# Kernel optimization log

Hardware: AMD Instinct MI355X
Metric: run time of the kernel (lower is better)

## Reference

```python
import jax, jax.numpy as jnp
import numpy as np

P, D, K, E, ITERS, THRESH, NCLS = 16, 384, 16, 8, 10, 0.9, 1000


def _forward(x, pw, pb, ln_g, ln_b, pos, qw, qb, kw, kb, vw, vb,
             ew, eb, nw, nb, m1w, m1b, m2w, m2b, fbw, fbb, fgw, fgb, cw, cb):
    B, C, H, W = x.shape
    Hp, Wp = H // P, W // P
    # patch embedding: conv(k=s=P) == reshape + matmul; (c, ph, pw) ordering matches conv weight layout
    xp = x.reshape(B, C, Hp, P, Wp, P).transpose(0, 2, 4, 1, 3, 5).reshape(B, Hp * Wp, C * P * P)
    patches = xp @ pw + pb                                    # [B, N, D]
    # layer norm (eps=1e-5)
    mu = patches.mean(-1, keepdims=True)
    var = patches.var(-1, keepdims=True)
    pn = (patches - mu) / jnp.sqrt(var + 1e-5) * ln_g + ln_b
    # k-means (Lloyd, fixed iters, deterministic evenly-spaced init)
    N = pn.shape[1]
    init_idx = jnp.linspace(0, N - 1, K).astype(jnp.int32)
    centers0 = pn[:, init_idx]                                # [B, K, D]
    pn_sq = jnp.sum(pn * pn, -1)                              # [B, N]

    def kstep(centers, _):
        d2 = (pn_sq[:, :, None]
              - 2.0 * jnp.einsum('bnd,bkd->bnk', pn, centers)
              + jnp.sum(centers * centers, -1)[:, None, :])   # [B, N, K]
        oh = jax.nn.one_hot(jnp.argmin(d2, -1), K, dtype=pn.dtype)
        counts = oh.sum(1)                                    # [B, K]
        new = jnp.einsum('bnk,bnd->bkd', oh, pn) / jnp.maximum(counts, 1.0)[:, :, None]
        new = jnp.where(counts[:, :, None] > 0, new, centers)
        return new, None

    clusters, _ = jax.lax.scan(kstep, centers0, None, length=ITERS)  # [B, K, D]
    # attention over clusters
    clusters = clusters + pos
    Q = clusters @ qw + qb
    Kt = clusters @ kw + kb
    V = clusters @ vw + vb
    attn = jax.nn.softmax(jnp.einsum('bqd,bkd->bqk', Q, Kt) / jnp.sqrt(jnp.float32(D)), -1)
    clusters = jnp.einsum('bqk,bkd->bqd', attn, V)
    # hypergraph laplacian
    hw = jax.nn.softmax(clusters @ ew + eb, axis=1)           # [B, K, E], softmax over nodes
    Dd = hw.sum(1)                                            # [B, E]
    Hm = hw.transpose(0, 2, 1)                                # [B, E, K]
    M = (Dd ** -0.5)[:, :, None] * Hm                         # D^{-1/2} H
    L = jnp.eye(E, dtype=clusters.dtype) - jnp.einsum('bek,bfk->bef', M, Hm)  # [B, E, E]
    L = jnp.pad(L, ((0, 0), (0, K - E), (0, K - E)))          # pad to [B, K, K]
    clusters = jnp.einsum('bij,bjd->bid', L, clusters)
    clusters = clusters @ nw + nb
    # non-linear propagation MLP (exact GELU, torch default)
    clusters = jax.nn.gelu(clusters @ m1w + m1b, approximate=False) @ m2w + m2b
    # adaptive node collapse: mask from ORIGINAL clusters, sequential in-place merges
    nrm = jnp.maximum(jnp.linalg.norm(clusters, axis=-1, keepdims=True), 1e-12)
    nc = clusters / nrm
    sim = jnp.einsum('bqd,bkd->bqk', nc, nc)
    mask_any = jnp.any(sim > THRESH, axis=0)                  # [K, K]: merge pair if ANY batch exceeds
    for i in range(K):                                        # small fixed K; matches sequential torch loop
        for j in range(i + 1, K):
            cond = mask_any[i, j]
            merged = (clusters[:, i] + clusters[:, j]) * 0.5
            clusters = clusters.at[:, i].set(jnp.where(cond, merged, clusters[:, i]))
            clusters = clusters.at[:, j].set(jnp.where(cond, merged, clusters[:, j]))
    # feedback modulation
    g = clusters.mean(1)                                      # [B, D]
    fb = g @ fbw + fbb
    gate = jax.nn.sigmoid(g @ fgw + fgb)                      # [B, 1]
    clusters = clusters + fb[:, None, :] * gate[:, None, :]
    return clusters.reshape(B, -1) @ cw + cb                  # [B, num_classes]


def setup_inputs() -> dict:
    key = jax.random.key(0)
    ks = jax.random.split(key, 16)
    Wm = lambda k, *s: jax.random.normal(k, s, jnp.float32) * 0.02
    z = lambda *s: jnp.zeros(s, jnp.float32)
    return {
        'x': jax.random.normal(ks[0], (128, 3, 224, 224), jnp.float32),
        'pw': Wm(ks[1], 3 * P * P, D), 'pb': z(D),
        'ln_g': jnp.ones((D,), jnp.float32), 'ln_b': z(D),
        'pos': Wm(ks[2], K, D),
        'qw': Wm(ks[3], D, D), 'qb': z(D),
        'kw': Wm(ks[4], D, D), 'kb': z(D),
        'vw': Wm(ks[5], D, D), 'vb': z(D),
        'ew': Wm(ks[6], D, E), 'eb': z(E),
        'nw': Wm(ks[7], D, D), 'nb': z(D),
        'm1w': Wm(ks[8], D, D), 'm1b': z(D),
        'm2w': Wm(ks[9], D, D), 'm2b': z(D),
        'fbw': Wm(ks[10], D, D), 'fbb': z(D),
        'fgw': Wm(ks[11], D, 1), 'fgb': z(1),
        'cw': Wm(ks[12], D * K, NCLS), 'cb': z(NCLS),
    }


def reference(x, pw, pb, ln_g, ln_b, pos, qw, qb, kw, kb, vw, vb,
              ew, eb, nw, nb, m1w, m1b, m2w, m2b, fbw, fbb, fgw, fgb, cw, cb):
    return _forward(x, pw, pb, ln_g, ln_b, pos, qw, qb, kw, kb, vw, vb,
                    ew, eb, nw, nb, m1w, m1b, m2w, m2b, fbw, fbb, fgw, fgb, cw, cb)
```

## Files before the change

kernel.cpp:

```cpp
#include <hip/hip_runtime.h>
#include <math.h>

#define NBATCH 128
#define NPTS   196
#define DIN    768
#define DM     384
#define KCL    16
#define NEXP   8
#define NITER  10
#define NCLS   1000

__global__ __launch_bounds__(256) void init_kernel(const float* __restrict__ cb,
                                                   float* __restrict__ out,
                                                   int* __restrict__ mask) {
    int idx = blockIdx.x * 256 + threadIdx.x;
    if (idx < NBATCH * NCLS) {
        out[idx] = cb[idx % NCLS];
    } else if (idx < NBATCH * NCLS + 256) {
        mask[idx - NBATCH * NCLS] = 0;
    }
}

#define BKP 16
__global__ __launch_bounds__(512, 4) void patch_ln_kernel(
        const float* __restrict__ x, const float* __restrict__ pw,
        const float* __restrict__ pb, const float* __restrict__ lng,
        const float* __restrict__ lnb, float* __restrict__ pn,
        float* __restrict__ pnsq) {
    __shared__ float As[BKP * 68];
    __shared__ float Ws[BKP * DM];
    const int tid = threadIdx.x;
    const int m0  = blockIdx.x * 64;
    const int rg  = tid >> 6;
    const int cg  = tid & 63;
    const int lr = (tid & 255) >> 2, kq = tid & 3;
    const int m  = m0 + lr;
    const int bi = m / NPTS, n = m - bi * NPTS;
    const int nh = n / 14, nwp = n - nh * 14;
    const float* xb = x + (size_t)bi * 150528 + (size_t)(nh * 16) * 224 + nwp * 16;

    float acc[8][6];
#pragma unroll
    for (int r = 0; r < 8; ++r)
#pragma unroll
        for (int j = 0; j < 6; ++j) acc[r][j] = 0.f;

    const float4* pw4 = (const float4*)pw;
    for (int kc = 0; kc < DIN; kc += BKP) {
        if (tid < 256) {
            int k = kc + kq * 4;
            int c = k >> 8, py = (k >> 4) & 15, px = k & 15;
            float4 xv = *(const float4*)(xb + c * 50176 + py * 224 + px);
            As[(kq * 4 + 0) * 68 + lr] = xv.x;
            As[(kq * 4 + 1) * 68 + lr] = xv.y;
            As[(kq * 4 + 2) * 68 + lr] = xv.z;
            As[(kq * 4 + 3) * 68 + lr] = xv.w;
        }
#pragma unroll
        for (int t = 0; t < 3; ++t) {
            int s = tid + t * 512;
            ((float4*)Ws)[s] = pw4[kc * 96 + s];
        }
        __syncthreads();
#pragma unroll 4
        for (int kk = 0; kk < BKP; ++kk) {
            float a[8];
            *(float4*)&a[0] = *(const float4*)&As[kk * 68 + rg * 8];
            *(float4*)&a[4] = *(const float4*)&As[kk * 68 + rg * 8 + 4];
            float w[6];
#pragma unroll
            for (int j = 0; j < 6; ++j) w[j] = Ws[kk * DM + cg + 64 * j];
#pragma unroll
            for (int r = 0; r < 8; ++r)
#pragma unroll
                for (int j = 0; j < 6; ++j) acc[r][j] += a[r] * w[j];
        }
        __syncthreads();
    }

    float gvv[6], bvv[6], pbv[6];
#pragma unroll
    for (int j = 0; j < 6; ++j) {
        pbv[j] = pb[cg + 64 * j];
        gvv[j] = lng[cg + 64 * j];
        bvv[j] = lnb[cg + 64 * j];
    }
#pragma unroll
    for (int r = 0; r < 8; ++r) {
        float vloc[6];
        float s = 0.f;
#pragma unroll
        for (int j = 0; j < 6; ++j) { vloc[j] = acc[r][j] + pbv[j]; s += vloc[j]; }
#pragma unroll
        for (int off = 32; off >= 1; off >>= 1) s += __shfl_xor(s, off);
        float mu = s * (1.0f / DM);
        float q = 0.f;
#pragma unroll
        for (int j = 0; j < 6; ++j) { float dd = vloc[j] - mu; q += dd * dd; }
#pragma unroll
        for (int off = 32; off >= 1; off >>= 1) q += __shfl_xor(q, off);
        float rstd = rsqrtf(q * (1.0f / DM) + 1e-5f);
        float ov[6];
        float ssq = 0.f;
#pragma unroll
        for (int j = 0; j < 6; ++j) {
            float p = (vloc[j] - mu) * rstd * gvv[j] + bvv[j];
            ov[j] = p; ssq += p * p;
        }
#pragma unroll
        for (int off = 32; off >= 1; off >>= 1) ssq += __shfl_xor(ssq, off);
        int mr = m0 + rg * 8 + r;
        float* dst = pn + (size_t)mr * DM + cg;
#pragma unroll
        for (int j = 0; j < 6; ++j) dst[64 * j] = ov[j];
        if (cg == 0) pnsq[mr] = ssq;
    }
}

__global__ __launch_bounds__(256) void kmeans_init_kernel(
        const float* __restrict__ pn, float* __restrict__ cent,
        float* __restrict__ csq, int* __restrict__ cnt) {
    const int b = blockIdx.x, tid = threadIdx.x;
    const float* pnb = pn + (size_t)b * NPTS * DM;
    float* cb = cent + (size_t)b * KCL * DM;
    for (int i = tid; i < KCL * DM / 4; i += 256) {
        int k = i / (DM / 4), d4 = i - k * (DM / 4);
        ((float4*)cb)[i] = ((const float4*)(pnb + (size_t)(13 * k) * DM))[d4];
    }
    if (tid < 128) {
        int k = tid >> 3, sub = tid & 7;
        const float* row = pnb + (size_t)(13 * k) * DM + sub * 48;
        float ss = 0.f;
        for (int d = 0; d < 48; d += 4) {
            float4 v = *(const float4*)(row + d);
            ss += v.x * v.x + v.y * v.y + v.z * v.z + v.w * v.w;
        }
#pragma unroll
        for (int off = 4; off >= 1; off >>= 1) ss += __shfl_xor(ss, off);
        if (sub == 0) csq[b * KCL + k] = ss;
    }
    if (tid < KCL) cnt[b * KCL + tid] = 0;
}

__global__ __launch_bounds__(256) void kmeans_assign_kernel(
        const float* __restrict__ pn, const float* __restrict__ pnsq,
        const float* __restrict__ cent, const float* __restrict__ csq,
        int* __restrict__ asn, int* __restrict__ cnt) {
    __shared__ float cs[KCL * DM];
    __shared__ float cq[KCL];
    const int b = blockIdx.y, tile = blockIdx.x, tid = threadIdx.x;
    const float* cb = cent + (size_t)b * KCL * DM;
    for (int i = tid; i < KCL * DM / 4; i += 256)
        ((float4*)cs)[i] = ((const float4*)cb)[i];
    if (tid < KCL) cq[tid] = csq[b * KCL + tid];
    __syncthreads();

    const int p = tid >> 3, sub = tid & 7;
    const int n = tile * 32 + p;
    if (n >= NPTS) return;
    const float4* prow = (const float4*)(pn + ((size_t)b * NPTS + n) * DM);

    float acc[KCL];
#pragma unroll
    for (int k = 0; k < KCL; ++k) acc[k] = 0.f;
#pragma unroll 2
    for (int i = 0; i < 12; ++i) {
        const int d4 = sub + 8 * i;
        float4 pv = prow[d4];
#pragma unroll
        for (int k = 0; k < KCL; ++k) {
            const float4 c = *(const float4*)&cs[k * DM + d4 * 4];
            acc[k] += pv.x * c.x + pv.y * c.y + pv.z * c.z + pv.w * c.w;
        }
    }
#pragma unroll
    for (int k = 0; k < KCL; ++k) {
        float a = acc[k];
        a += __shfl_xor(a, 1);
        a += __shfl_xor(a, 2);
        a += __shfl_xor(a, 4);
        acc[k] = a;
    }
    if (sub == 0) {
        const float mp = pnsq[b * NPTS + n];
        float best = (mp - 2.0f * acc[0]) + cq[0];
        int bk = 0;
#pragma unroll
        for (int k = 1; k < KCL; ++k) {
            float v = (mp - 2.0f * acc[k]) + cq[k];
            if (v < best) { best = v; bk = k; }
        }
        asn[b * NPTS + n] = bk;
        atomicAdd(&cnt[b * KCL + bk], 1);
    }
}

__global__ __launch_bounds__(256) void kmeans_update_kernel(
        const float* __restrict__ pn, const int* __restrict__ asn,
        int* __restrict__ cnt, float* __restrict__ cent,
        float* __restrict__ csq) {
    __shared__ unsigned long long msk[4];
    __shared__ float red[4];
    const int b = blockIdx.y, k = blockIdx.x, tid = threadIdx.x;

    int a = -1;
    if (tid < NPTS) a = asn[b * NPTS + tid];
    unsigned long long bal = __ballot(a == k);
    if ((tid & 63) == 0) msk[tid >> 6] = bal;
    __syncthreads();

    const int c = cnt[b * KCL + k];
    float sx = 0.f, sy = 0.f;
    const float* pnb = pn + (size_t)b * NPTS * DM + 2 * tid;
    if (tid < 192) {
#pragma unroll
        for (int w = 0; w < 4; ++w) {
            unsigned long long m = msk[w];
            while (m) {
                int nn = w * 64 + (int)__builtin_ctzll(m);
                m &= m - 1;
                float2 v = *(const float2*)(pnb + (size_t)nn * DM);
                sx += v.x; sy += v.y;
            }
        }
    }
    float* cr = cent + ((size_t)b * KCL + k) * DM + 2 * tid;
    float nx = 0.f, ny = 0.f;
    if (tid < 192) {
        if (c > 0) {
            float inv = 1.0f / (float)c;
            nx = sx * inv; ny = sy * inv;
        } else {
            nx = cr[0]; ny = cr[1];
        }
        cr[0] = nx; cr[1] = ny;
    }
    float ss = nx * nx + ny * ny;
#pragma unroll
    for (int off = 32; off >= 1; off >>= 1) ss += __shfl_xor(ss, off);
    if ((tid & 63) == 0) red[tid >> 6] = ss;
    __syncthreads();
    if (tid == 0) {
        csq[b * KCL + k] = red[0] + red[1] + red[2] + red[3];
        cnt[b * KCL + k] = 0;
    }
}

__global__ __launch_bounds__(256) void kmeans_finalize_kernel(
        float* __restrict__ cent, const float* __restrict__ pos) {
    int i = blockIdx.x * 256 + threadIdx.x;
    int within = i % (KCL * DM / 4);
    float4 cv = ((const float4*)cent)[i];
    float4 pv = ((const float4*)pos)[within];
    cv.x += pv.x; cv.y += pv.y; cv.z += pv.z; cv.w += pv.w;
    ((float4*)cent)[i] = cv;
}

__global__ __launch_bounds__(256) void gemm_qkv_kernel(
        const float* __restrict__ A,
        const float* __restrict__ qw, const float* __restrict__ kw,
        const float* __restrict__ vw,
        const float* __restrict__ qb, const float* __restrict__ kb,
        const float* __restrict__ vb,
        float* __restrict__ Q, float* __restrict__ K, float* __restrict__ V) {
    __shared__ float As[32 * 32];
    __shared__ float Ws[3][32 * 128];
    const int n0 = blockIdx.x * 128;
    const int m0 = blockIdx.y * 32;
    const int tid = threadIdx.x;
    const int rg = tid >> 5, cg = tid & 31;
    const int arow = tid >> 3, akg = tid & 7;
    const float* W[3] = {qw, kw, vw};

    float acc[3][4][4];
#pragma unroll
    for (int g = 0; g < 3; ++g)
#pragma unroll
        for (int r = 0; r < 4; ++r)
#pragma unroll
            for (int j = 0; j < 4; ++j) acc[g][r][j] = 0.f;

    for (int kc = 0; kc < DM; kc += 32) {
        float4 av = *(const float4*)(A + (size_t)(m0 + arow) * DM + kc + akg * 4);
        As[(akg * 4 + 0) * 32 + arow] = av.x;
        As[(akg * 4 + 1) * 32 + arow] = av.y;
        As[(akg * 4 + 2) * 32 + arow] = av.z;
        As[(akg * 4 + 3) * 32 + arow] = av.w;
#pragma unroll
        for (int g = 0; g < 3; ++g)
#pragma unroll
            for (int t = 0; t < 4; ++t) {
                int s = tid + t * 256;
                int kk = s >> 5, c4i = s & 31;
                *(float4*)&Ws[g][kk * 128 + c4i * 4] =
                    *(const float4*)(W[g] + (size_t)(kc + kk) * DM + n0 + c4i * 4);
            }
        __syncthreads();
#pragma unroll 8
        for (int kk = 0; kk < 32; ++kk) {
            float4 a = *(const float4*)&As[kk * 32 + rg * 4];
            float ar[4] = {a.x, a.y, a.z, a.w};
#pragma unroll
            for (int g = 0; g < 3; ++g) {
                float4 w = *(const float4*)&Ws[g][kk * 128 + cg * 4];
                float wr[4] = {w.x, w.y, w.z, w.w};
#pragma unroll
                for (int r = 0; r < 4; ++r)
#pragma unroll
                    for (int j = 0; j < 4; ++j) acc[g][r][j] += ar[r] * wr[j];
            }
        }
        __syncthreads();
    }
    const float* B[3] = {qb, kb, vb};
    float* O[3] = {Q, K, V};
#pragma unroll
    for (int g = 0; g < 3; ++g) {
        float4 bv = *(const float4*)(B[g] + n0 + cg * 4);
        float bvr[4] = {bv.x, bv.y, bv.z, bv.w};
#pragma unroll
        for (int r = 0; r < 4; ++r) {
            float o[4];
#pragma unroll
            for (int j = 0; j < 4; ++j) o[j] = acc[g][r][j] + bvr[j];
            *(float4*)(O[g] + (size_t)(m0 + rg * 4 + r) * DM + n0 + cg * 4) =
                *(float4*)&o[0];
        }
    }
}

template <int ACT>
__global__ __launch_bounds__(256) void gemm_kernel(
        const float* __restrict__ A, const float* __restrict__ W,
        const float* __restrict__ bias, float* __restrict__ out,
        int M, int N, int Kd) {
    __shared__ float As[32 * 32];
    __shared__ float Ws[32 * 128];
    const int n0 = blockIdx.x * 128;
    const int m0 = blockIdx.y * 32;
    const int tid = threadIdx.x;
    const int rg = tid >> 5, cg = tid & 31;
    const int arow = tid >> 3, akg = tid & 7;
    float acc[4][4];
#pragma unroll
    for (int r = 0; r < 4; ++r)
#pragma unroll
        for (int j = 0; j < 4; ++j) acc[r][j] = 0.f;

    for (int kc = 0; kc < Kd; kc += 32) {
        float4 av = *(const float4*)(A + (size_t)(m0 + arow) * Kd + kc + akg * 4);
        As[(akg * 4 + 0) * 32 + arow] = av.x;
        As[(akg * 4 + 1) * 32 + arow] = av.y;
        As[(akg * 4 + 2) * 32 + arow] = av.z;
        As[(akg * 4 + 3) * 32 + arow] = av.w;
#pragma unroll
        for (int t = 0; t < 4; ++t) {
            int s = tid + t * 256;
            int kk = s >> 5, c4i = s & 31;
            *(float4*)&Ws[kk * 128 + c4i * 4] =
                *(const float4*)(W + (size_t)(kc + kk) * N + n0 + c4i * 4);
        }
        __syncthreads();
#pragma unroll 16
        for (int kk = 0; kk < 32; ++kk) {
            float4 a = *(const float4*)&As[kk * 32 + rg * 4];
            float4 w = *(const float4*)&Ws[kk * 128 + cg * 4];
            float ar[4] = {a.x, a.y, a.z, a.w};
            float wr[4] = {w.x, w.y, w.z, w.w};
#pragma unroll
            for (int r = 0; r < 4; ++r)
#pragma unroll
                for (int j = 0; j < 4; ++j) acc[r][j] += ar[r] * wr[j];
        }
        __syncthreads();
    }
    float4 bv = *(const float4*)(bias + n0 + cg * 4);
    float bvr[4] = {bv.x, bv.y, bv.z, bv.w};
#pragma unroll
    for (int r = 0; r < 4; ++r) {
        float o[4];
#pragma unroll
        for (int j = 0; j < 4; ++j) {
            float v = acc[r][j] + bvr[j];
            if (ACT == 1) v = 0.5f * v * (1.0f + erff(v * 0.70710678118654752440f));
            o[j] = v;
        }
        *(float4*)(out + (size_t)(m0 + rg * 4 + r) * N + n0 + cg * 4) = *(float4*)&o[0];
    }
}

__global__ __launch_bounds__(256) void attn_spectral_kernel(
        const float* __restrict__ Qg, const float* __restrict__ Kg,
        const float* __restrict__ Vg, const float* __restrict__ ew,
        const float* __restrict__ eb, float* __restrict__ c2) {
    __shared__ float Qs[KCL * 388];
    __shared__ float Ks[KCL * 388];
    __shared__ float ewt[NEXP * 388];
    __shared__ float Ss[KCL * 17];
    __shared__ float hws[KCL * 9];
    __shared__ float rds[NEXP];
    __shared__ float Ls[NEXP * NEXP];
    const int b = blockIdx.x, tid = threadIdx.x;
    for (int idx = tid; idx < KCL * DM; idx += 256) {
        int i = idx / DM, d = idx - i * DM;
        size_t g = (size_t)b * KCL * DM + idx;
        Qs[i * 388 + d] = Qg[g];
        Ks[i * 388 + d] = Kg[g];
    }
    for (int idx = tid; idx < DM * NEXP; idx += 256) {
        int d = idx >> 3, e = idx & 7;
        ewt[e * 388 + d] = ew[idx];
    }
    __syncthreads();
    {
        int i = tid >> 4, j = tid & 15;
        float acc = 0.f;
        for (int d = 0; d < DM; d += 4) {
            float4 q = *(const float4*)&Qs[i * 388 + d];
            float4 k = *(const float4*)&Ks[j * 388 + d];
            acc += q.x * k.x + q.y * k.y + q.z * k.z + q.w * k.w;
        }
        float s = acc / sqrtf((float)DM);
        float mx = s;
#pragma unroll
        for (int off = 8; off >= 1; off >>= 1) mx = fmaxf(mx, __shfl_xor(mx, off));
        float p = expf(s - mx);
        float sm = p;
#pragma unroll
        for (int off = 8; off >= 1; off >>= 1) sm += __shfl_xor(sm, off);
        Ss[i * 17 + j] = p / sm;
    }
    __syncthreads();
    for (int idx = tid; idx < KCL * DM; idx += 256) {
        int i = idx / DM, d = idx - i * DM;
        Ks[i * 388 + d] = Vg[(size_t)b * KCL * DM + idx];
    }
    __syncthreads();
    for (int idx = tid; idx < KCL * DM; idx += 256) {
        int i = idx / DM, d = idx - i * DM;
        float acc = 0.f;
#pragma unroll
        for (int j = 0; j < KCL; ++j) acc += Ss[i * 17 + j] * Ks[j * 388 + d];
        Qs[i * 388 + d] = acc;
    }
    __syncthreads();
    if (tid < 128) {
        int e = tid >> 4, i = tid & 15;
        float l = 0.f;
        for (int d4 = 0; d4 < DM / 4; ++d4) {
            float4 q = *(const float4*)&Qs[i * 388 + d4 * 4];
            float4 w = *(const float4*)&ewt[e * 388 + d4 * 4];
            l += q.x * w.x + q.y * w.y + q.z * w.z + q.w * w.w;
        }
        l += eb[e];
        float mx = l;
#pragma unroll
        for (int off = 8; off >= 1; off >>= 1) mx = fmaxf(mx, __shfl_xor(mx, off));
        float p = expf(l - mx);
        float sm = p;
#pragma unroll
        for (int off = 8; off >= 1; off >>= 1) sm += __shfl_xor(sm, off);
        float h = p / sm;
        hws[i * 9 + e] = h;
        float sd = h;
#pragma unroll
        for (int off = 8; off >= 1; off >>= 1) sd += __shfl_xor(sd, off);
        if (i == 0) rds[e] = 1.0f / sqrtf(sd);
    }
    __syncthreads();
    if (tid < 64) {
        int e = tid >> 3, f = tid & 7;
        float gsum = 0.f;
#pragma unroll
        for (int k = 0; k < KCL; ++k) gsum += hws[k * 9 + e] * hws[k * 9 + f];
        Ls[e * 8 + f] = ((e == f) ? 1.0f : 0.0f) - rds[e] * gsum;
    }
    __syncthreads();
    for (int idx = tid; idx < KCL * DM; idx += 256) {
        int i = idx / DM, d = idx - i * DM;
        float acc = 0.f;
        if (i < NEXP) {
#pragma unroll
            for (int j = 0; j < NEXP; ++j) acc += Ls[i * 8 + j] * Qs[j * 388 + d];
        }
        c2[(size_t)b * KCL * DM + idx] = acc;
    }
}

__global__ __launch_bounds__(256) void simmask_kernel(const float* __restrict__ c4,
                                                      int* __restrict__ mask) {
    __shared__ float Cs[KCL * 388];
    __shared__ float rns[KCL];
    const int b = blockIdx.x, tid = threadIdx.x;
    for (int idx = tid; idx < KCL * DM; idx += 256) {
        int i = idx / DM, d = idx - i * DM;
        Cs[i * 388 + d] = c4[(size_t)b * KCL * DM + idx];
    }
    __syncthreads();
    {
        int i = tid >> 4, s = tid & 15;
        float ss = 0.f;
        for (int t = 0; t < 24; ++t) { float v = Cs[i * 388 + s + 16 * t]; ss += v * v; }
#pragma unroll
        for (int off = 8; off >= 1; off >>= 1) ss += __shfl_xor(ss, off);
        if (s == 0) rns[i] = 1.0f / fmaxf(sqrtf(ss), 1e-12f);
    }
    __syncthreads();
    for (int idx = tid; idx < KCL * DM; idx += 256) {
        int i = idx / DM, d = idx - i * DM;
        Cs[i * 388 + d] *= rns[i];
    }
    __syncthreads();
    {
        int i = tid >> 4, j = tid & 15;
        if (j > i) {
            float dp = 0.f;
            for (int d = 0; d < DM; d += 4) {
                float4 a = *(const float4*)&Cs[i * 388 + d];
                float4 c = *(const float4*)&Cs[j * 388 + d];
                dp += a.x * c.x + a.y * c.y + a.z * c.z + a.w * c.w;
            }
            if (dp > 0.9f) atomicOr(&mask[i * KCL + j], 1);
        }
    }
}

__global__ __launch_bounds__(256) void merge_fb_kernel(
        const float* __restrict__ c4, const int* __restrict__ mask,
        const float* __restrict__ fbw, const float* __restrict__ fbb,
        const float* __restrict__ fgw, const float* __restrict__ fgb,
        float* __restrict__ c5) {
    __shared__ int   mk[256];
    __shared__ float gs[DM];
    __shared__ float wred[3];
    __shared__ float gatev;
    const int b = blockIdx.x, tid = threadIdx.x;
    mk[tid] = mask[tid];
    const bool act = tid < 192;
    const int t = tid;
    float2 v[KCL];
    if (act) {
#pragma unroll
        for (int i = 0; i < KCL; ++i)
            v[i] = *(const float2*)(c4 + (size_t)b * KCL * DM + i * DM + 2 * t);
    }
    __syncthreads();
    if (act) {
#pragma unroll
        for (int i = 0; i < KCL; ++i)
#pragma unroll
            for (int j = i + 1; j < KCL; ++j)
                if (mk[i * KCL + j]) {
                    float mx = 0.5f * (v[i].x + v[j].x);
                    float my = 0.5f * (v[i].y + v[j].y);
                    v[i].x = mx; v[i].y = my; v[j].x = mx; v[j].y = my;
                }
    }
    float2 gv = {0.f, 0.f};
    if (act) {
#pragma unroll
        for (int i = 0; i < KCL; ++i) { gv.x += v[i].x; gv.y += v[i].y; }
        gv.x *= 0.0625f; gv.y *= 0.0625f;
        gs[2 * t] = gv.x; gs[2 * t + 1] = gv.y;
    }
    float pg = act ? (gv.x * fgw[2 * t] + gv.y * fgw[2 * t + 1]) : 0.f;
#pragma unroll
    for (int off = 32; off >= 1; off >>= 1) pg += __shfl_xor(pg, off);
    if (act && (tid & 63) == 0) wred[tid >> 6] = pg;
    __syncthreads();
    if (tid == 0) {
        float d = wred[0] + wred[1] + wred[2] + fgb[0];
        gatev = 1.0f / (1.0f + expf(-d));
    }
    __syncthreads();
    if (act) {
        float fx = fbb[2 * t], fy = fbb[2 * t + 1];
        for (int j = 0; j < DM; ++j) {
            float gj = gs[j];
            const float2 w = *(const float2*)(fbw + (size_t)j * DM + 2 * t);
            fx += gj * w.x; fy += gj * w.y;
        }
        float gt = gatev;
#pragma unroll
        for (int i = 0; i < KCL; ++i) {
            float2 o = {v[i].x + fx * gt, v[i].y + fy * gt};
            *(float2*)(c5 + (size_t)b * KCL * DM + i * DM + 2 * t) = o;
        }
    }
}

__global__ __launch_bounds__(256) void cls_kernel(const float* __restrict__ A,
                                                  const float* __restrict__ Wt,
                                                  float* __restrict__ out) {
    __shared__ float As[32 * 32];
    __shared__ float Ws[32 * 128];
    const int n0 = blockIdx.x * 128;
    const int m0 = blockIdx.y * 32;
    const int k0 = blockIdx.z * 768;
    const int tid = threadIdx.x;
    const int rg = tid >> 5, cg = tid & 31;
    const int arow = tid >> 3, akg = tid & 7;
    float acc[4][4];
#pragma unroll
    for (int r = 0; r < 4; ++r)
#pragma unroll
        for (int j = 0; j < 4; ++j) acc[r][j] = 0.f;

    for (int kc = k0; kc < k0 + 768; kc += 32) {
        float4 av = *(const float4*)(A + (size_t)(m0 + arow) * (KCL * DM) + kc + akg * 4);
        As[(akg * 4 + 0) * 32 + arow] = av.x;
        As[(akg * 4 + 1) * 32 + arow] = av.y;
        As[(akg * 4 + 2) * 32 + arow] = av.z;
        As[(akg * 4 + 3) * 32 + arow] = av.w;
#pragma unroll
        for (int ti = 0; ti < 4; ++ti) {
            int s = tid + ti * 256;
            int kk = s >> 5, c4i = s & 31;
            int col = n0 + c4i * 4;
            float4 wv = make_float4(0.f, 0.f, 0.f, 0.f);
            if (col < NCLS) wv = *(const float4*)(Wt + (size_t)(kc + kk) * NCLS + col);
            *(float4*)&Ws[kk * 128 + c4i * 4] = wv;
        }
        __syncthreads();
#pragma unroll 16
        for (int kk = 0; kk < 32; ++kk) {
            float4 a = *(const float4*)&As[kk * 32 + rg * 4];
            float4 w = *(const float4*)&Ws[kk * 128 + cg * 4];
            float ar[4] = {a.x, a.y, a.z, a.w};
            float wr[4] = {w.x, w.y, w.z, w.w};
#pragma unroll
            for (int r = 0; r < 4; ++r)
#pragma unroll
                for (int j = 0; j < 4; ++j) acc[r][j] += ar[r] * wr[j];
        }
        __syncthreads();
    }
    int col = n0 + cg * 4;
    if (col < NCLS) {
#pragma unroll
        for (int r = 0; r < 4; ++r) {
            int row = m0 + rg * 4 + r;
#pragma unroll
            for (int j = 0; j < 4; ++j)
                atomicAdd(&out[(size_t)row * NCLS + col + j], acc[r][j]);
        }
    }
}

extern "C" void kernel_launch(void* const* d_in, const int* in_sizes, int n_in,
                              void* d_out, int out_size, void* d_ws, size_t ws_size,
                              hipStream_t stream) {
    const float* x   = (const float*)d_in[0];
    const float* pw  = (const float*)d_in[1];
    const float* pb  = (const float*)d_in[2];
    const float* lng = (const float*)d_in[3];
    const float* lnb = (const float*)d_in[4];
    const float* pos = (const float*)d_in[5];
    const float* qw  = (const float*)d_in[6];
    const float* qb  = (const float*)d_in[7];
    const float* kw  = (const float*)d_in[8];
    const float* kb  = (const float*)d_in[9];
    const float* vw  = (const float*)d_in[10];
    const float* vb  = (const float*)d_in[11];
    const float* ew  = (const float*)d_in[12];
    const float* eb  = (const float*)d_in[13];
    const float* nw  = (const float*)d_in[14];
    const float* nb  = (const float*)d_in[15];
    const float* m1w = (const float*)d_in[16];
    const float* m1b = (const float*)d_in[17];
    const float* m2w = (const float*)d_in[18];
    const float* m2b = (const float*)d_in[19];
    const float* fbw = (const float*)d_in[20];
    const float* fbb = (const float*)d_in[21];
    const float* fgw = (const float*)d_in[22];
    const float* fgb = (const float*)d_in[23];
    const float* cw  = (const float*)d_in[24];
    const float* cb  = (const float*)d_in[25];
    float* out = (float*)d_out;
    float* ws  = (float*)d_ws;

    float* pn_   = ws;
    float* pnsq_ = ws + 9633792;
    float* c0_   = ws + 9658880;
    float* Q_    = ws + 10445312;
    float* K_    = ws + 11231744;
    float* V_    = ws + 12018176;
    float* c2_   = ws + 12804608;
    int*   mask_ = (int*)(ws + 13591040);
    float* csq_  = ws + 13591296;
    int*   cnt_  = (int*)(ws + 13593344);
    int*   asn_  = (int*)(ws + 13595392);
    float* cent_ = c0_;
    float* c3_ = Q_;
    float* h_  = K_;
    float* c4_ = V_;
    float* c5_ = c0_;

    init_kernel<<<501, 256, 0, stream>>>(cb, out, mask_);
    patch_ln_kernel<<<392, 512, 0, stream>>>(x, pw, pb, lng, lnb, pn_, pnsq_);

    kmeans_init_kernel<<<NBATCH, 256, 0, stream>>>(pn_, cent_, csq_, cnt_);
    for (int it = 0; it < NITER; ++it) {
        kmeans_assign_kernel<<<dim3(7, NBATCH), 256, 0, stream>>>(
            pn_, pnsq_, cent_, csq_, asn_, cnt_);
        kmeans_update_kernel<<<dim3(KCL, NBATCH), 256, 0, stream>>>(
            pn_, asn_, cnt_, cent_, csq_);
    }
    kmeans_finalize_kernel<<<768, 256, 0, stream>>>(cent_, pos);

    gemm_qkv_kernel<<<dim3(3, 64), 256, 0, stream>>>(c0_, qw, kw, vw, qb, kb, vb,
                                                     Q_, K_, V_);
    attn_spectral_kernel<<<NBATCH, 256, 0, stream>>>(Q_, K_, V_, ew, eb, c2_);
    gemm_kernel<0><<<dim3(3, 64), 256, 0, stream>>>(c2_, nw, nb, c3_, 2048, DM, DM);
    gemm_kernel<1><<<dim3(3, 64), 256, 0, stream>>>(c3_, m1w, m1b, h_, 2048, DM, DM);
    gemm_kernel<0><<<dim3(3, 64), 256, 0, stream>>>(h_, m2w, m2b, c4_, 2048, DM, DM);
    simmask_kernel<<<NBATCH, 256, 0, stream>>>(c4_, mask_);
    merge_fb_kernel<<<NBATCH, 256, 0, stream>>>(c4_, mask_, fbw, fbb, fgw, fgb, c5_);
    cls_kernel<<<dim3(8, 4, 8), 256, 0, stream>>>(c5_, cw, out);
}
```

Before: 987.9 us.

## Fuse k-means init, iterations and finalize into one persistent per-batch kernel

Replaces the init, ten assign/update kernel pairs and the finalize kernel with a single kernel that runs one 1024-thread block per batch. Centers, their squared norms and the assignments stay in shared memory across all iterations. This removes about 22 kernel launches, the global atomics and the round trips of centers through global memory. In exchange only 128 blocks run, each computing two points per thread and reloading points from global/L2 on every iteration, so the GPU may be underused.

```diff
diff --git a/kernel.cpp b/kernel.cpp
--- a/kernel.cpp
+++ b/kernel.cpp
@@ -117,143 +117,139 @@
     }
 }
 
-__global__ __launch_bounds__(256) void kmeans_init_kernel(
-        const float* __restrict__ pn, float* __restrict__ cent,
-        float* __restrict__ csq, int* __restrict__ cnt) {
-    const int b = blockIdx.x, tid = threadIdx.x;
-    const float* pnb = pn + (size_t)b * NPTS * DM;
-    float* cb = cent + (size_t)b * KCL * DM;
-    for (int i = tid; i < KCL * DM / 4; i += 256) {
-        int k = i / (DM / 4), d4 = i - k * (DM / 4);
-        ((float4*)cb)[i] = ((const float4*)(pnb + (size_t)(13 * k) * DM))[d4];
-    }
-    if (tid < 128) {
-        int k = tid >> 3, sub = tid & 7;
-        const float* row = pnb + (size_t)(13 * k) * DM + sub * 48;
-        float ss = 0.f;
-        for (int d = 0; d < 48; d += 4) {
-            float4 v = *(const float4*)(row + d);
-            ss += v.x * v.x + v.y * v.y + v.z * v.z + v.w * v.w;
-        }
-#pragma unroll
-        for (int off = 4; off >= 1; off >>= 1) ss += __shfl_xor(ss, off);
-        if (sub == 0) csq[b * KCL + k] = ss;
-    }
-    if (tid < KCL) cnt[b * KCL + tid] = 0;
-}
-
-__global__ __launch_bounds__(256) void kmeans_assign_kernel(
+#define RED8(v) { v += __shfl_xor(v, 1); v += __shfl_xor(v, 2); \
+                  v += __shfl_xor(v, 4); }
+
+__global__ __launch_bounds__(1024) void kmeans_fused_kernel(
         const float* __restrict__ pn, const float* __restrict__ pnsq,
-        const float* __restrict__ cent, const float* __restrict__ csq,
-        int* __restrict__ asn, int* __restrict__ cnt) {
+        const float* __restrict__ pos, float* __restrict__ c0) {
     __shared__ float cs[KCL * DM];
     __shared__ float cq[KCL];
-    const int b = blockIdx.y, tile = blockIdx.x, tid = threadIdx.x;
-    const float* cb = cent + (size_t)b * KCL * DM;
-    for (int i = tid; i < KCL * DM / 4; i += 256)
-        ((float4*)cs)[i] = ((const float4*)cb)[i];
-    if (tid < KCL) cq[tid] = csq[b * KCL + tid];
-    __syncthreads();
+    __shared__ float spq[NPTS];
+    __shared__ int   asn[256];
+    const int b = blockIdx.x, tid = threadIdx.x;
+    const float4* pn4 = (const float4*)(pn + (size_t)b * NPTS * DM);
+    float4* cs4 = (float4*)cs;
+
+    for (int idx = tid; idx < KCL * DM / 4; idx += 1024) {
+        int k = idx / 96, d4 = idx - k * 96;
+        cs4[idx] = pn4[(size_t)(13 * k) * 96 + d4];
+    }
+    if (tid < NPTS) spq[tid] = pnsq[b * NPTS + tid];
+    if (tid >= NPTS && tid < 256) asn[tid] = -1;
+    __syncthreads();
+    {
+        const int w = tid >> 6, lane = tid & 63;
+        float4 A = cs4[w * 96 + lane];
+        float ss = A.x * A.x + A.y * A.y + A.z * A.z + A.w * A.w;
+        if (lane < 32) {
+            float4 B = cs4[w * 96 + 64 + lane];
+            ss += B.x * B.x + B.y * B.y + B.z * B.z + B.w * B.w;
+        }
+#pragma unroll
+        for (int off = 32; off >= 1; off >>= 1) ss += __shfl_xor(ss, off);
+        if (lane == 0) cq[w] = ss;
+    }
 
     const int p = tid >> 3, sub = tid & 7;
-    const int n = tile * 32 + p;
-    if (n >= NPTS) return;
-    const float4* prow = (const float4*)(pn + ((size_t)b * NPTS + n) * DM);
-
-    float acc[KCL];
-#pragma unroll
-    for (int k = 0; k < KCL; ++k) acc[k] = 0.f;
+    const int p2 = p + 128;
+    const bool v2 = (p2 < NPTS);
+    const int p2c = v2 ? p2 : 0;
+    for (int it = 0; it < NITER; ++it) {
+        __syncthreads();
+        float acc0[KCL], acc1[KCL];
+#pragma unroll
+        for (int k = 0; k < KCL; ++k) { acc0[k] = 0.f; acc1[k] = 0.f; }
 #pragma unroll 2
-    for (int i = 0; i < 12; ++i) {
-        const int d4 = sub + 8 * i;
-        float4 pv = prow[d4];
+        for (int i = 0; i < 12; ++i) {
+            const int d4 = sub + 8 * i;
+            float4 a0 = pn4[(size_t)p * 96 + d4];
+            float4 a1 = pn4[(size_t)p2c * 96 + d4];
+#pragma unroll
+            for (int k = 0; k < KCL; ++k) {
+                float4 c = *(const float4*)&cs[k * DM + d4 * 4];
+                acc0[k] += a0.x * c.x + a0.y * c.y + a0.z * c.z + a0.w * c.w;
+                acc1[k] += a1.x * c.x + a1.y * c.y + a1.z * c.z + a1.w * c.w;
+            }
+        }
 #pragma unroll
         for (int k = 0; k < KCL; ++k) {
-            const float4 c = *(const float4*)&cs[k * DM + d4 * 4];
-            acc[k] += pv.x * c.x + pv.y * c.y + pv.z * c.z + pv.w * c.w;
-        }
-    }
-#pragma unroll
-    for (int k = 0; k < KCL; ++k) {
-        float a = acc[k];
-        a += __shfl_xor(a, 1);
-        a += __shfl_xor(a, 2);
-        a += __shfl_xor(a, 4);
-        acc[k] = a;
-    }
-    if (sub == 0) {
-        const float mp = pnsq[b * NPTS + n];
-        float best = (mp - 2.0f * acc[0]) + cq[0];
-        int bk = 0;
-#pragma unroll
-        for (int k = 1; k < KCL; ++k) {
-            float v = (mp - 2.0f * acc[k]) + cq[k];
-            if (v < best) { best = v; bk = k; }
-        }
-        asn[b * NPTS + n] = bk;
-        atomicAdd(&cnt[b * KCL + bk], 1);
-    }
-}
-
-__global__ __launch_bounds__(256) void kmeans_update_kernel(
-        const float* __restrict__ pn, const int* __restrict__ asn,
-        int* __restrict__ cnt, float* __restrict__ cent,
-        float* __restrict__ csq) {
-    __shared__ unsigned long long msk[4];
-    __shared__ float red[4];
-    const int b = blockIdx.y, k = blockIdx.x, tid = threadIdx.x;
-
-    int a = -1;
-    if (tid < NPTS) a = asn[b * NPTS + tid];
-    unsigned long long bal = __ballot(a == k);
-    if ((tid & 63) == 0) msk[tid >> 6] = bal;
-    __syncthreads();
-
-    const int c = cnt[b * KCL + k];
-    float sx = 0.f, sy = 0.f;
-    const float* pnb = pn + (size_t)b * NPTS * DM + 2 * tid;
-    if (tid < 192) {
-#pragma unroll
-        for (int w = 0; w < 4; ++w) {
-            unsigned long long m = msk[w];
-            while (m) {
-                int nn = w * 64 + (int)__builtin_ctzll(m);
-                m &= m - 1;
-                float2 v = *(const float2*)(pnb + (size_t)nn * DM);
-                sx += v.x; sy += v.y;
+            float a = acc0[k]; RED8(a); acc0[k] = a;
+            float d = acc1[k]; RED8(d); acc1[k] = d;
+        }
+        if (sub == 0) {
+            {
+                float mp = spq[p];
+                float best = (mp - 2.0f * acc0[0]) + cq[0]; int bk = 0;
+#pragma unroll
+                for (int k = 1; k < KCL; ++k) {
+                    float v = (mp - 2.0f * acc0[k]) + cq[k];
+                    if (v < best) { best = v; bk = k; }
+                }
+                asn[p] = bk;
             }
-        }
-    }
-    float* cr = cent + ((size_t)b * KCL + k) * DM + 2 * tid;
-    float nx = 0.f, ny = 0.f;
-    if (tid < 192) {
-        if (c > 0) {
-            float inv = 1.0f / (float)c;
-            nx = sx * inv; ny = sy * inv;
-        } else {
-            nx = cr[0]; ny = cr[1];
-        }
-        cr[0] = nx; cr[1] = ny;
-    }
-    float ss = nx * nx + ny * ny;
-#pragma unroll
-    for (int off = 32; off >= 1; off >>= 1) ss += __shfl_xor(ss, off);
-    if ((tid & 63) == 0) red[tid >> 6] = ss;
-    __syncthreads();
-    if (tid == 0) {
-        csq[b * KCL + k] = red[0] + red[1] + red[2] + red[3];
-        cnt[b * KCL + k] = 0;
-    }
-}
-
-__global__ __launch_bounds__(256) void kmeans_finalize_kernel(
-        float* __restrict__ cent, const float* __restrict__ pos) {
-    int i = blockIdx.x * 256 + threadIdx.x;
-    int within = i % (KCL * DM / 4);
-    float4 cv = ((const float4*)cent)[i];
-    float4 pv = ((const float4*)pos)[within];
-    cv.x += pv.x; cv.y += pv.y; cv.z += pv.z; cv.w += pv.w;
-    ((float4*)cent)[i] = cv;
+            if (v2) {
+                float mp = spq[p2];
+                float best = (mp - 2.0f * acc1[0]) + cq[0]; int bk = 0;
+#pragma unroll
+                for (int k = 1; k < KCL; ++k) {
+                    float v = (mp - 2.0f * acc1[k]) + cq[k];
+                    if (v < best) { best = v; bk = k; }
+                }
+                asn[p2] = bk;
+            }
+        }
+        __syncthreads();
+        {
+            const int w = tid >> 6, lane = tid & 63;
+            float4 sA = make_float4(0.f, 0.f, 0.f, 0.f);
+            float4 sB = make_float4(0.f, 0.f, 0.f, 0.f);
+            int c = 0;
+#pragma unroll
+            for (int ch = 0; ch < 4; ++ch) {
+                int a = asn[ch * 64 + lane];
+                unsigned long long m = __ballot(a == w);
+                c += __popcll(m);
+                while (m) {
+                    int nn = ch * 64 + (int)__builtin_ctzll(m);
+                    m &= m - 1;
+                    float4 vA = pn4[(size_t)nn * 96 + lane];
+                    sA.x += vA.x; sA.y += vA.y; sA.z += vA.z; sA.w += vA.w;
+                    if (lane < 32) {
+                        float4 vB = pn4[(size_t)nn * 96 + 64 + lane];
+                        sB.x += vB.x; sB.y += vB.y; sB.z += vB.z; sB.w += vB.w;
+                    }
+                }
+            }
+            float4 nA, nB = make_float4(0.f, 0.f, 0.f, 0.f);
+            if (c > 0) {
+                float inv = 1.0f / (float)c;
+                nA.x = sA.x * inv; nA.y = sA.y * inv; nA.z = sA.z * inv; nA.w = sA.w * inv;
+                if (lane < 32) {
+                    nB.x = sB.x * inv; nB.y = sB.y * inv; nB.z = sB.z * inv; nB.w = sB.w * inv;
+                }
+            } else {
+                nA = cs4[w * 96 + lane];
+                if (lane < 32) nB = cs4[w * 96 + 64 + lane];
+            }
+            cs4[w * 96 + lane] = nA;
+            if (lane < 32) cs4[w * 96 + 64 + lane] = nB;
+            float ss = nA.x * nA.x + nA.y * nA.y + nA.z * nA.z + nA.w * nA.w
+                     + nB.x * nB.x + nB.y * nB.y + nB.z * nB.z + nB.w * nB.w;
+#pragma unroll
+            for (int off = 32; off >= 1; off >>= 1) ss += __shfl_xor(ss, off);
+            if (lane == 0) cq[w] = ss;
+        }
+    }
+    __syncthreads();
+    const float4* pos4 = (const float4*)pos;
+    float4* c0b = (float4*)(c0 + (size_t)b * KCL * DM);
+    for (int idx = tid; idx < KCL * DM / 4; idx += 1024) {
+        float4 cv = cs4[idx];
+        float4 pv = pos4[idx];
+        cv.x += pv.x; cv.y += pv.y; cv.z += pv.z; cv.w += pv.w;
+        c0b[idx] = cv;
+    }
 }
 
 __global__ __launch_bounds__(256) void gemm_qkv_kernel(
@@ -687,10 +683,6 @@
     float* V_    = ws + 12018176;
     float* c2_   = ws + 12804608;
     int*   mask_ = (int*)(ws + 13591040);
-    float* csq_  = ws + 13591296;
-    int*   cnt_  = (int*)(ws + 13593344);
-    int*   asn_  = (int*)(ws + 13595392);
-    float* cent_ = c0_;
     float* c3_ = Q_;
     float* h_  = K_;
     float* c4_ = V_;
@@ -699,14 +691,7 @@
     init_kernel<<<501, 256, 0, stream>>>(cb, out, mask_);
     patch_ln_kernel<<<392, 512, 0, stream>>>(x, pw, pb, lng, lnb, pn_, pnsq_);
 
-    kmeans_init_kernel<<<NBATCH, 256, 0, stream>>>(pn_, cent_, csq_, cnt_);
-    for (int it = 0; it < NITER; ++it) {
-        kmeans_assign_kernel<<<dim3(7, NBATCH), 256, 0, stream>>>(
-            pn_, pnsq_, cent_, csq_, asn_, cnt_);
-        kmeans_update_kernel<<<dim3(KCL, NBATCH), 256, 0, stream>>>(
-            pn_, asn_, cnt_, cent_, csq_);
-    }
-    kmeans_finalize_kernel<<<768, 256, 0, stream>>>(cent_, pos);
+    kmeans_fused_kernel<<<NBATCH, 1024, 0, stream>>>(pn_, pnsq_, pos, c0_);
 
     gemm_qkv_kernel<<<dim3(3, 64), 256, 0, stream>>>(c0_, qw, kw, vw, qb, kb, vb,
                                                      Q_, K_, V_);
```

Result: faster. 965.5 us (-2.3%).
